# Optimization experiments

Measured on AMD Instinct MI355X. Metric: run time of the kernel, lower is better.

Reference implementation:

```python
import jax, jax.numpy as jnp
import numpy as np

LATENT = 64  # latent_size -> N = K = LATENT**2 = 4096 codes/tokens


def setup_inputs() -> dict:
    key = jax.random.key(0)
    k1, k2 = jax.random.split(key)
    hidden, L = 1024, LATENT
    z = jax.random.normal(k1, (hidden, L, L), dtype=jnp.float32)
    code_books = jax.random.uniform(k2, (hidden, L, L), dtype=jnp.float32)  # torch.rand init
    return {"z": z, "code_books": code_books}


def reference(z, code_books):
    # z, code_books: (D=hidden, L, L). Tokens/codes are columns of the flattened maps.
    D = z.shape[0]
    zf = z.reshape(D, -1).T           # (N, D) tokens
    cb = code_books.reshape(D, -1).T  # (K, D) codebook entries
    # Squared L2 distance via GEMM trick: ||a-b||^2 = ||a||^2 + ||b||^2 - 2 a.b
    # (avoids the N x K x D broadcast intermediate of the original)
    d2 = (jnp.sum(zf * zf, axis=1)[:, None]
          + jnp.sum(cb * cb, axis=1)[None, :]
          - 2.0 * zf @ cb.T)          # (N, K)
    idx = jnp.argmin(d2, axis=1)      # (N,)
    zq = cb[idx]                      # (N, D) gather
    zq = zq.reshape(LATENT, LATENT, -1).transpose(2, 0, 1)  # (D, L, L)
    # Straight-through: z = zq + (z - zq).detach()  (z was detached before lookup)
    z_st = zq + jax.lax.stop_gradient(z - zq)
    return z_st, zq
```

## Files before the change

### kernel.cpp

```cpp
#include <hip/hip_runtime.h>
#include <stdint.h>

#define D  1024
#define NK 4096
#define KA 1024
#define KB 1024
#define BK 32
#define NT (KA / BK)
#define TAU 0.15f
#define CW  0.12f
#define MAXC 1024

typedef __attribute__((ext_vector_type(8))) _Float16 f16x8;
typedef __attribute__((ext_vector_type(4))) float f32x4;
typedef unsigned long long u64;

__device__ __forceinline__ uint32_t fkey(float f) {
    uint32_t b = __float_as_uint(f);
    return (b & 0x80000000u) ? ~b : (b | 0x80000000u);
}
__device__ __forceinline__ float unfkey(uint32_t u) {
    uint32_t b = (u & 0x80000000u) ? (u & 0x7fffffffu) : ~u;
    return __uint_as_float(b);
}
__device__ __forceinline__ u64 umin64(u64 a, u64 b) { return a < b ? a : b; }
__device__ __forceinline__ u64 umax64(u64 a, u64 b) { return a > b ? a : b; }

__device__ __forceinline__ void gload16(void* lds, const void* g) {
    __builtin_amdgcn_global_load_lds(
        (const __attribute__((address_space(1))) unsigned int*)g,
        (__attribute__((address_space(3))) unsigned int*)lds, 16, 0, 0);
}

__global__ void cbnorm_kernel(const float* __restrict__ cb, float* __restrict__ cbn) {
    __shared__ float red[256];
    const int kk = threadIdx.x & 63;
    const int dc = threadIdx.x >> 6;
    const int k  = blockIdx.x * 64 + kk;
    float s = 0.f;
    for (int d = dc; d < D; d += 4) {
        float v = cb[d * NK + k];
        s = fmaf(v, v, s);
    }
    red[threadIdx.x] = s;
    __syncthreads();
    if (dc == 0) cbn[k] = (red[kk] + red[64 + kk]) + (red[128 + kk] + red[192 + kk]);
}

__global__ __launch_bounds__(256) void split_transpose(
        const float* __restrict__ z, const float* __restrict__ cb,
        _Float16* __restrict__ Ap, _Float16* __restrict__ Bp,
        float* __restrict__ partial) {
    __shared__ float T[64][65];
    const int isZ = (blockIdx.z == 0);
    const float* src = isZ ? z : cb;
    _Float16* dst = isZ ? Ap : Bp;
    const int n0 = blockIdx.x * 64, d0 = blockIdx.y * 64;
    const int t = threadIdx.x;
#pragma unroll
    for (int i = 0; i < 4; ++i) {
        int dl = (t >> 4) + i * 16;
        int nl = (t & 15) * 4;
        float4 v = *(const float4*)&src[(size_t)(d0 + dl) * NK + n0 + nl];
        T[dl][nl] = v.x; T[dl][nl + 1] = v.y; T[dl][nl + 2] = v.z; T[dl][nl + 3] = v.w;
    }
    __syncthreads();
    const int nr = t >> 2, dch = (t & 3) * 16;
    f16x8 h0, h1;
    float s = 0.f;
#pragma unroll
    for (int j = 0; j < 8; ++j) {
        float v = T[dch + j][nr];
        s = fmaf(v, v, s);
        h0[j] = (_Float16)v;
    }
#pragma unroll
    for (int j = 0; j < 8; ++j) {
        float v = T[dch + 8 + j][nr];
        s = fmaf(v, v, s);
        h1[j] = (_Float16)v;
    }
    size_t base = (size_t)(n0 + nr) * KA + d0 + dch;
    *(f16x8*)&dst[base]     = h0;
    *(f16x8*)&dst[base + 8] = h1;
    if (!isZ) {
        s += __shfl_xor(s, 1);
        s += __shfl_xor(s, 2);
        if ((t & 3) == 0) partial[(size_t)(d0 >> 6) * NK + n0 + nr] = s;
    }
}

__global__ void cbnorm_finish(const float* __restrict__ partial, float* __restrict__ cbn) {
    const int k = blockIdx.x * 256 + threadIdx.x;
    float s = 0.f;
#pragma unroll
    for (int j = 0; j < 16; ++j) s += partial[(size_t)j * NK + k];
    cbn[k] = s;
}

__global__ __launch_bounds__(256) void gemm_mfma(
        const _Float16* __restrict__ Ap, const _Float16* __restrict__ Bp,
        const float* __restrict__ cbn, ulonglong2* __restrict__ tp) {
    __shared__ _Float16 As[128 * 32];
    __shared__ _Float16 Bs[128 * 32];
    const int tid = threadIdx.x;
    const int xcd = blockIdx.x & 7, idx = blockIdx.x >> 3;
    const int n0 = (((xcd >> 2) * 16) + (idx >> 3)) * 128;
    const int k0 = (((xcd & 3) * 8) + (idx & 7)) * 128;
    const int w = tid >> 6, l = tid & 63;
    const int wr = w >> 1, wc = w & 1;
    const int fr = l & 15, fq = l >> 4;

    f32x4 acc[4][4] = {};

    const int srow = tid >> 2;
    const int swz = (((tid & 3) ^ ((tid >> 3) & 3)) * 8);
    const _Float16* gA0 = Ap + (size_t)(n0 + srow) * KA + swz;
    const _Float16* gA1 = Ap + (size_t)(n0 + 64 + srow) * KA + swz;
    const _Float16* gB0 = Bp + (size_t)(k0 + srow) * KB + swz;
    const _Float16* gB1 = Bp + (size_t)(k0 + 64 + srow) * KB + swz;

    const int rcol = (fq ^ ((fr >> 1) & 3)) * 8;

    for (int kt = 0; kt < NT; ++kt) {
        const size_t ka = (size_t)kt * BK;
        gload16(&As[tid * 8],        gA0 + ka);
        gload16(&As[2048 + tid * 8], gA1 + ka);
        gload16(&Bs[tid * 8],        gB0 + ka);
        gload16(&Bs[2048 + tid * 8], gB1 + ka);
        __syncthreads();
        f16x8 a[4], bb[4];
#pragma unroll
        for (int mi = 0; mi < 4; ++mi)
            a[mi] = *(const f16x8*)&As[(wr * 64 + mi * 16 + fr) * 32 + rcol];
#pragma unroll
        for (int ni = 0; ni < 4; ++ni)
            bb[ni] = *(const f16x8*)&Bs[(wc * 64 + ni * 16 + fr) * 32 + rcol];
#pragma unroll
        for (int mi = 0; mi < 4; ++mi)
#pragma unroll
            for (int ni = 0; ni < 4; ++ni)
                acc[mi][ni] = __builtin_amdgcn_mfma_f32_16x16x32_f16(a[mi], bb[ni], acc[mi][ni], 0, 0, 0);
        __syncthreads();
    }

    float cbv[4];
#pragma unroll
    for (int ni = 0; ni < 4; ++ni) cbv[ni] = cbn[k0 + wc * 64 + ni * 16 + fr];
    const int kt64 = (k0 / 64) + wc;
#pragma unroll
    for (int mi = 0; mi < 4; ++mi) {
#pragma unroll
        for (int reg = 0; reg < 4; ++reg) {
            u64 b1 = ~0ull, b2 = ~0ull;
#pragma unroll
            for (int ni = 0; ni < 4; ++ni) {
                float s = cbv[ni] - 2.f * acc[mi][ni][reg];
                u64 p = ((u64)fkey(s) << 32) | (unsigned)(k0 + wc * 64 + ni * 16 + fr);
                if (p < b1) { b2 = b1; b1 = p; } else if (p < b2) b2 = p;
            }
#pragma unroll
            for (int m = 8; m >= 1; m >>= 1) {
                u64 q1 = __shfl_xor(b1, m);
                u64 q2 = __shfl_xor(b2, m);
                u64 nb1 = umin64(b1, q1);
                u64 nb2 = umin64(umax64(b1, q1), umin64(b2, q2));
                b1 = nb1; b2 = nb2;
            }
            if (fr == 0) {
                int n = n0 + wr * 64 + mi * 16 + fq * 4 + reg;
                ulonglong2 v; v.x = b1; v.y = b2;
                tp[(size_t)kt64 * NK + n] = v;
            }
        }
    }
}

__global__ __launch_bounds__(256) void reduce_rows(
        const ulonglong2* __restrict__ tp, int* __restrict__ idx,
        int* __restrict__ rescue, u64* __restrict__ rbest, int* __restrict__ ctr) {
    __shared__ ulonglong2 sh[4][64];
    const int no = threadIdx.x & 63, st = threadIdx.x >> 6;
    const int n = blockIdx.x * 64 + no;
    u64 b1 = ~0ull, b2 = ~0ull;
#pragma unroll 4
    for (int g = st * 16; g < st * 16 + 16; ++g) {
        ulonglong2 e = tp[(size_t)g * NK + n];
        u64 nb1 = umin64(b1, e.x);
        u64 nb2 = umin64(umax64(b1, e.x), umin64(b2, e.y));
        b1 = nb1; b2 = nb2;
    }
    ulonglong2 v; v.x = b1; v.y = b2;
    sh[st][no] = v;
    __syncthreads();
    if (st == 0) {
#pragma unroll
        for (int j = 1; j < 4; ++j) {
            ulonglong2 e = sh[j][no];
            u64 nb1 = umin64(b1, e.x);
            u64 nb2 = umin64(umax64(b1, e.x), umin64(b2, e.y));
            b1 = nb1; b2 = nb2;
        }
        idx[n] = (int)(b1 & 0xffffffffull);
        float f1 = unfkey((uint32_t)(b1 >> 32));
        float f2 = unfkey((uint32_t)(b2 >> 32));
        if (f2 - f1 < TAU) {
            int p = atomicAdd(ctr, 1);
            rescue[p] = n;
            rbest[p] = ~0ull;
        }
    }
}

__global__ __launch_bounds__(256) void rescue_kernel(
        const float* __restrict__ z, const float* __restrict__ cb,
        const float* __restrict__ cbn, const ulonglong2* __restrict__ tp,
        const int* __restrict__ rescue, const int* __restrict__ ctr,
        u64* __restrict__ rbest) {
    const int cnt = min(*ctr, NK);
    const int slot = blockIdx.x;
    if (slot >= cnt) return;
    const int n = rescue[slot];
    const int tid = threadIdx.x;
    const int lane = tid & 63, wv = tid >> 6;

    __shared__ float zn[D];
    __shared__ int cand[MAXC];
    __shared__ int ccnt, overflow;
    __shared__ u64 wred[4];

    if (tid == 0) { ccnt = 0; overflow = 0; }
    for (int d = tid; d < D; d += 256) zn[d] = z[(size_t)d * NK + n];

    if (tid < 64) {
        ulonglong2 e = tp[(size_t)tid * NK + n];
        u64 m = e.x;
#pragma unroll
        for (int msk = 32; msk >= 1; msk >>= 1) m = umin64(m, __shfl_xor(m, msk));
        const float thr = unfkey((uint32_t)(m >> 32)) + CW;
        if (unfkey((uint32_t)(e.y >> 32)) < thr) {
            int p = atomicAdd(&ccnt, 64);
            if (p + 64 <= MAXC) {
                for (int j = 0; j < 64; ++j) cand[p + j] = tid * 64 + j;
            } else overflow = 1;
        } else if (unfkey((uint32_t)(e.x >> 32)) < thr) {
            int p = atomicAdd(&ccnt, 1);
            if (p < MAXC) cand[p] = (int)(e.x & 0xffffffffull);
            else overflow = 1;
        }
    }
    __syncthreads();

    const int ovf = overflow;
    const int m = ovf ? NK : min(ccnt, MAXC);
    u64 best = ~0ull;
    for (int ci = wv; ci < m; ci += 4) {
        const int k = ovf ? ci : cand[ci];
        float s = 0.f;
#pragma unroll
        for (int j = 0; j < 16; ++j)
            s = fmaf(zn[lane + j * 64], cb[(size_t)(lane + j * 64) * NK + k], s);
#pragma unroll
        for (int msk = 32; msk >= 1; msk >>= 1) s += __shfl_xor(s, msk);
        float sc = cbn[k] - 2.f * s;
        best = umin64(best, ((u64)fkey(sc) << 32) | (unsigned)k);
    }
    if (lane == 0) wred[wv] = best;
    __syncthreads();
    if (tid == 0)
        rbest[slot] = umin64(umin64(wred[0], wred[1]), umin64(wred[2], wred[3]));
}

__global__ void fix_idx(const int* __restrict__ rescue, const int* __restrict__ ctr,
                        const u64* __restrict__ rbest, int* __restrict__ idx) {
    const int cnt = min(*ctr, NK);
    for (int s = threadIdx.x + blockIdx.x * 256; s < cnt; s += gridDim.x * 256)
        idx[rescue[s]] = (int)(rbest[s] & 0xffffffffull);
}

__global__ __launch_bounds__(256) void gemm_argmin(
        const float* __restrict__ z, const float* __restrict__ cb,
        const float* __restrict__ cbn, unsigned long long* __restrict__ best) {
    __shared__ float Zs[8][128];
    __shared__ float Cs[8][128];
    const int n0 = blockIdx.y * 128, k0 = blockIdx.x * 128;
    const int tid = threadIdx.x;
    const int tx = tid & 15, ty = tid >> 4;
    const int lr = tid >> 5, lc = (tid & 31) << 2;
    float acc[8][8];
#pragma unroll
    for (int i = 0; i < 8; ++i)
#pragma unroll
        for (int j = 0; j < 8; ++j) acc[i][j] = 0.f;
    for (int d0 = 0; d0 < D; d0 += 8) {
        float4 zv = *(const float4*)&z [(d0 + lr) * NK + n0 + lc];
        float4 cv = *(const float4*)&cb[(d0 + lr) * NK + k0 + lc];
        __syncthreads();
        *(float4*)&Zs[lr][lc] = zv;
        *(float4*)&Cs[lr][lc] = cv;
        __syncthreads();
#pragma unroll
        for (int dd = 0; dd < 8; ++dd) {
            float4 a0 = *(const float4*)&Zs[dd][ty * 8];
            float4 a1 = *(const float4*)&Zs[dd][ty * 8 + 4];
            float4 b0 = *(const float4*)&Cs[dd][tx * 8];
            float4 b1 = *(const float4*)&Cs[dd][tx * 8 + 4];
            float a[8] = {a0.x, a0.y, a0.z, a0.w, a1.x, a1.y, a1.z, a1.w};
            float b[8] = {b0.x, b0.y, b0.z, b0.w, b1.x, b1.y, b1.z, b1.w};
#pragma unroll
            for (int i = 0; i < 8; ++i)
#pragma unroll
                for (int j = 0; j < 8; ++j) acc[i][j] = fmaf(a[i], b[j], acc[i][j]);
        }
    }
    float cbnv[8];
#pragma unroll
    for (int j = 0; j < 8; ++j) cbnv[j] = cbn[k0 + tx * 8 + j];
#pragma unroll
    for (int i = 0; i < 8; ++i) {
        float bv = cbnv[0] - 2.f * acc[i][0];
        int bj = 0;
#pragma unroll
        for (int j = 1; j < 8; ++j) {
            float v = cbnv[j] - 2.f * acc[i][j];
            if (v < bv) { bv = v; bj = j; }
        }
        u64 p = ((u64)fkey(bv) << 32) | (unsigned)(k0 + tx * 8 + bj);
#pragma unroll
        for (int m = 8; m >= 1; m >>= 1) {
            u64 q = __shfl_xor(p, m);
            if (q < p) p = q;
        }
        if (tx == 0) atomicMin(&best[n0 + ty * 8 + i], p);
    }
}

__global__ void extract_idx(const unsigned long long* __restrict__ best,
                            int* __restrict__ idx) {
    int n = blockIdx.x * 256 + threadIdx.x;
    idx[n] = (int)(unsigned)(best[n] & 0xFFFFFFFFull);
}

__global__ void gather_kernel(const float* __restrict__ z, const float* __restrict__ cb,
                              const int* __restrict__ idx, float* __restrict__ out) {
    const int d = blockIdx.x;
    const float* cbrow = &cb[(size_t)d * NK];
    const float* zrow  = &z [(size_t)d * NK];
    float* st = &out[(size_t)d * NK];
    float* zq = &out[(size_t)D * NK + (size_t)d * NK];
    for (int n4 = threadIdx.x; n4 < NK / 4; n4 += 256) {
        int4 iv = *(const int4*)&idx[n4 * 4];
        float4 zv = *(const float4*)&zrow[n4 * 4];
        float4 q;
        q.x = cbrow[iv.x]; q.y = cbrow[iv.y]; q.z = cbrow[iv.z]; q.w = cbrow[iv.w];
        float4 stv;
        stv.x = q.x + (zv.x - q.x);
        stv.y = q.y + (zv.y - q.y);
        stv.z = q.z + (zv.z - q.z);
        stv.w = q.w + (zv.w - q.w);
        *(float4*)&st[n4 * 4] = stv;
        *(float4*)&zq[n4 * 4] = q;
    }
}

extern "C" void kernel_launch(void* const* d_in, const int* in_sizes, int n_in,
                              void* d_out, int out_size, void* d_ws, size_t ws_size,
                              hipStream_t stream) {
    const float* z  = (const float*)d_in[0];
    const float* cb = (const float*)d_in[1];
    float* out = (float*)d_out;
    char* ws = (char*)d_ws;

    const size_t oA  = 0;
    const size_t oB  = oA + (size_t)NK * KA * 2;
    const size_t oT  = oB + (size_t)NK * KB * 2;
    const size_t oC  = oT + (size_t)NK * 64 * 16;
    const size_t oI  = oC + NK * 4;
    const size_t oR  = oI + NK * 4;
    const size_t oRB = oR + NK * 4;
    const size_t oN  = oRB + NK * 8;
    const size_t oP  = oN + 256;
    const size_t REQ = oP + (size_t)16 * NK * 4;

    if (ws_size >= REQ) {
        _Float16* Ap = (_Float16*)(ws + oA);
        _Float16* Bp = (_Float16*)(ws + oB);
        ulonglong2* tp = (ulonglong2*)(ws + oT);
        float* cbn = (float*)(ws + oC);
        int* idx = (int*)(ws + oI);
        int* rescue = (int*)(ws + oR);
        u64* rbest = (u64*)(ws + oRB);
        int* ctr = (int*)(ws + oN);
        float* partial = (float*)(ws + oP);

        hipMemsetAsync(ctr, 0, 4, stream);
        split_transpose<<<dim3(NK / 64, D / 64, 2), 256, 0, stream>>>(z, cb, Ap, Bp, partial);
        cbnorm_finish<<<16, 256, 0, stream>>>(partial, cbn);
        gemm_mfma<<<1024, 256, 0, stream>>>(Ap, Bp, cbn, tp);
        reduce_rows<<<64, 256, 0, stream>>>(tp, idx, rescue, rbest, ctr);
        rescue_kernel<<<4096, 256, 0, stream>>>(z, cb, cbn, tp, rescue, ctr, rbest);
        fix_idx<<<4, 256, 0, stream>>>(rescue, ctr, rbest, idx);
        gather_kernel<<<1024, 256, 0, stream>>>(z, cb, idx, out);
    } else {
        unsigned long long* best = (unsigned long long*)ws;
        float* cbn = (float*)(ws + NK * 8);
        int* idx = (int*)(ws + NK * 8 + NK * 4);
        hipMemsetAsync(best, 0xFF, NK * 8, stream);
        cbnorm_kernel<<<64, 256, 0, stream>>>(cb, cbn);
        gemm_argmin<<<dim3(NK / 128, NK / 128), 256, 0, stream>>>(z, cb, cbn, best);
        extract_idx<<<16, 256, 0, stream>>>(best, idx);
        gather_kernel<<<1024, 256, 0, stream>>>(z, cb, idx, out);
    }
}
```

Before: 96.04 us.

## Enlarge GEMM tiles to 256x256 with 4-stage LDS prefetch pipeline

The distance GEMM moves from 128x128 tiles with 256 threads to 256x256 tiles with 512 threads. Global-to-LDS loads are issued two stages ahead into a four-buffer ring, using explicit waitcnt, barriers and setprio so loads overlap the MFMA work. The per-tile top-2 selection now runs on float values with a separate index instead of packed 64-bit keys, and the second-best entry's index is dropped. In exchange, larger tiles raise LDS (64KB) and register pressure and cut the grid to 256 blocks. The manual vmcnt/barrier logic also needs care to stay correct.

```diff
diff --git a/kernel.cpp b/kernel.cpp
--- a/kernel.cpp
+++ b/kernel.cpp
@@ -5,11 +5,13 @@
 #define NK 4096
 #define KA 1024
 #define KB 1024
-#define BK 32
-#define NT (KA / BK)
 #define TAU 0.15f
 #define CW  0.12f
 #define MAXC 1024
+
+#define BK2 32
+#define NT2 (KA / BK2)
+#define NBUF 4
 
 typedef __attribute__((ext_vector_type(8))) _Float16 f16x8;
 typedef __attribute__((ext_vector_type(4))) float f32x4;
@@ -98,78 +100,124 @@
     cbn[k] = s;
 }
 
-__global__ __launch_bounds__(256) void gemm_mfma(
+__global__ __launch_bounds__(512, 2) void gemm_mfma(
         const _Float16* __restrict__ Ap, const _Float16* __restrict__ Bp,
         const float* __restrict__ cbn, ulonglong2* __restrict__ tp) {
-    __shared__ _Float16 As[128 * 32];
-    __shared__ _Float16 Bs[128 * 32];
+    __shared__ _Float16 As[NBUF][256 * BK2];
+    __shared__ _Float16 Bs[NBUF][256 * BK2];
     const int tid = threadIdx.x;
     const int xcd = blockIdx.x & 7, idx = blockIdx.x >> 3;
-    const int n0 = (((xcd >> 2) * 16) + (idx >> 3)) * 128;
-    const int k0 = (((xcd & 3) * 8) + (idx & 7)) * 128;
+    const int n0 = ((xcd >> 1) * 4 + (idx >> 3)) * 256;
+    const int k0 = ((xcd & 1) * 8 + (idx & 7)) * 256;
     const int w = tid >> 6, l = tid & 63;
-    const int wr = w >> 1, wc = w & 1;
+    const int wr = w >> 2, wc = w & 3;
     const int fr = l & 15, fq = l >> 4;
 
-    f32x4 acc[4][4] = {};
+    f32x4 acc[8][4] = {};
 
     const int srow = tid >> 2;
-    const int swz = (((tid & 3) ^ ((tid >> 3) & 3)) * 8);
+    const int swz = ((tid & 3) ^ ((tid >> 3) & 3)) * 8;
     const _Float16* gA0 = Ap + (size_t)(n0 + srow) * KA + swz;
-    const _Float16* gA1 = Ap + (size_t)(n0 + 64 + srow) * KA + swz;
+    const _Float16* gA1 = Ap + (size_t)(n0 + 128 + srow) * KA + swz;
     const _Float16* gB0 = Bp + (size_t)(k0 + srow) * KB + swz;
-    const _Float16* gB1 = Bp + (size_t)(k0 + 64 + srow) * KB + swz;
-
+    const _Float16* gB1 = Bp + (size_t)(k0 + 128 + srow) * KB + swz;
     const int rcol = (fq ^ ((fr >> 1) & 3)) * 8;
 
-    for (int kt = 0; kt < NT; ++kt) {
-        const size_t ka = (size_t)kt * BK;
-        gload16(&As[tid * 8],        gA0 + ka);
-        gload16(&As[2048 + tid * 8], gA1 + ka);
-        gload16(&Bs[tid * 8],        gB0 + ka);
-        gload16(&Bs[2048 + tid * 8], gB1 + ka);
-        __syncthreads();
-        f16x8 a[4], bb[4];
+    gload16(&As[0][tid * 8],        gA0);
+    gload16(&As[0][4096 + tid * 8], gA1);
+    gload16(&Bs[0][tid * 8],        gB0);
+    gload16(&Bs[0][4096 + tid * 8], gB1);
+    gload16(&As[1][tid * 8],        gA0 + BK2);
+    gload16(&As[1][4096 + tid * 8], gA1 + BK2);
+    gload16(&Bs[1][tid * 8],        gB0 + BK2);
+    gload16(&Bs[1][4096 + tid * 8], gB1 + BK2);
+    asm volatile("s_waitcnt vmcnt(4)" ::: "memory");
+    __builtin_amdgcn_s_barrier();
+    asm volatile("" ::: "memory");
+
+    for (int t = 0; t < NT2; ++t) {
+        const int b = t & 3;
+        const int pb = (t + 2) & 3;
+        const _Float16* Ab = As[b];
+        const _Float16* Bb = Bs[b];
+        const bool st = (t + 2) < NT2;
+
+        f16x8 bbf[4], a0[4];
+#pragma unroll
+        for (int ni = 0; ni < 4; ++ni)
+            bbf[ni] = *(const f16x8*)&Bb[(wc * 64 + ni * 16 + fr) * BK2 + rcol];
 #pragma unroll
         for (int mi = 0; mi < 4; ++mi)
-            a[mi] = *(const f16x8*)&As[(wr * 64 + mi * 16 + fr) * 32 + rcol];
-#pragma unroll
-        for (int ni = 0; ni < 4; ++ni)
-            bb[ni] = *(const f16x8*)&Bs[(wc * 64 + ni * 16 + fr) * 32 + rcol];
+            a0[mi] = *(const f16x8*)&Ab[(wr * 128 + mi * 16 + fr) * BK2 + rcol];
+        if (st) {
+            gload16(&As[pb][tid * 8],        gA0 + (t + 2) * BK2);
+            gload16(&As[pb][4096 + tid * 8], gA1 + (t + 2) * BK2);
+        }
+        __builtin_amdgcn_s_setprio(1);
 #pragma unroll
         for (int mi = 0; mi < 4; ++mi)
 #pragma unroll
             for (int ni = 0; ni < 4; ++ni)
-                acc[mi][ni] = __builtin_amdgcn_mfma_f32_16x16x32_f16(a[mi], bb[ni], acc[mi][ni], 0, 0, 0);
-        __syncthreads();
+                acc[mi][ni] = __builtin_amdgcn_mfma_f32_16x16x32_f16(a0[mi], bbf[ni], acc[mi][ni], 0, 0, 0);
+        __builtin_amdgcn_s_setprio(0);
+        __builtin_amdgcn_s_barrier();
+
+        f16x8 a1[4];
+#pragma unroll
+        for (int mi = 0; mi < 4; ++mi)
+            a1[mi] = *(const f16x8*)&Ab[(wr * 128 + 64 + mi * 16 + fr) * BK2 + rcol];
+        if (st) {
+            gload16(&Bs[pb][tid * 8],        gB0 + (t + 2) * BK2);
+            gload16(&Bs[pb][4096 + tid * 8], gB1 + (t + 2) * BK2);
+        }
+        __builtin_amdgcn_s_setprio(1);
+#pragma unroll
+        for (int mi = 0; mi < 4; ++mi)
+#pragma unroll
+            for (int ni = 0; ni < 4; ++ni)
+                acc[4 + mi][ni] = __builtin_amdgcn_mfma_f32_16x16x32_f16(a1[mi], bbf[ni], acc[4 + mi][ni], 0, 0, 0);
+        __builtin_amdgcn_s_setprio(0);
+
+        if (t < NT2 - 2) {
+            asm volatile("s_waitcnt vmcnt(4)" ::: "memory");
+        } else if (t == NT2 - 2) {
+            asm volatile("s_waitcnt vmcnt(0)" ::: "memory");
+        }
+        if (t < NT2 - 1) {
+            __builtin_amdgcn_s_barrier();
+            asm volatile("" ::: "memory");
+        }
     }
 
     float cbv[4];
 #pragma unroll
     for (int ni = 0; ni < 4; ++ni) cbv[ni] = cbn[k0 + wc * 64 + ni * 16 + fr];
-    const int kt64 = (k0 / 64) + wc;
-#pragma unroll
-    for (int mi = 0; mi < 4; ++mi) {
+    const int kt64 = (k0 >> 6) + wc;
+#pragma unroll
+    for (int mi = 0; mi < 8; ++mi) {
 #pragma unroll
         for (int reg = 0; reg < 4; ++reg) {
-            u64 b1 = ~0ull, b2 = ~0ull;
+            float b1f = 1e30f, b2f = 1e30f;
+            int b1k = 0;
 #pragma unroll
             for (int ni = 0; ni < 4; ++ni) {
-                float s = cbv[ni] - 2.f * acc[mi][ni][reg];
-                u64 p = ((u64)fkey(s) << 32) | (unsigned)(k0 + wc * 64 + ni * 16 + fr);
-                if (p < b1) { b2 = b1; b1 = p; } else if (p < b2) b2 = p;
+                float s = fmaf(-2.f, acc[mi][ni][reg], cbv[ni]);
+                b2f = fminf(fmaxf(s, b1f), b2f);
+                if (s < b1f) { b1f = s; b1k = k0 + wc * 64 + ni * 16 + fr; }
             }
 #pragma unroll
             for (int m = 8; m >= 1; m >>= 1) {
-                u64 q1 = __shfl_xor(b1, m);
-                u64 q2 = __shfl_xor(b2, m);
-                u64 nb1 = umin64(b1, q1);
-                u64 nb2 = umin64(umax64(b1, q1), umin64(b2, q2));
-                b1 = nb1; b2 = nb2;
+                float q1 = __shfl_xor(b1f, m);
+                int   qk = __shfl_xor(b1k, m);
+                float q2 = __shfl_xor(b2f, m);
+                b2f = fminf(fminf(b2f, q2), fmaxf(b1f, q1));
+                if (q1 < b1f) { b1f = q1; b1k = qk; }
             }
             if (fr == 0) {
-                int n = n0 + wr * 64 + mi * 16 + fq * 4 + reg;
-                ulonglong2 v; v.x = b1; v.y = b2;
+                int n = n0 + wr * 128 + mi * 16 + fq * 4 + reg;
+                ulonglong2 v;
+                v.x = ((u64)fkey(b1f) << 32) | (unsigned)b1k;
+                v.y = ((u64)fkey(b2f) << 32) | 0xffffffffu;
                 tp[(size_t)kt64 * NK + n] = v;
             }
         }
@@ -396,7 +444,7 @@
         hipMemsetAsync(ctr, 0, 4, stream);
         split_transpose<<<dim3(NK / 64, D / 64, 2), 256, 0, stream>>>(z, cb, Ap, Bp, partial);
         cbnorm_finish<<<16, 256, 0, stream>>>(partial, cbn);
-        gemm_mfma<<<1024, 256, 0, stream>>>(Ap, Bp, cbn, tp);
+        gemm_mfma<<<256, 512, 0, stream>>>(Ap, Bp, cbn, tp);
         reduce_rows<<<64, 256, 0, stream>>>(tp, idx, rescue, rbest, ctr);
         rescue_kernel<<<4096, 256, 0, stream>>>(z, cb, cbn, tp, rescue, ctr, rbest);
         fix_idx<<<4, 256, 0, stream>>>(rescue, ctr, rbest, idx);
```

Result: faster. 87.95 us (-8.4%).
